# Optimization experiments

Hardware: AMD Instinct MI355X
Metric: run time of the kernel (lower is better)

Reference implementation:

```python
import jax, jax.numpy as jnp
import numpy as np

EPS = 1e-5

def _ste(x, q):
    # straight-through estimator: forward=q, backward=identity
    return x + jax.lax.stop_gradient(q - x)

def act_quant(x):
    # per-token int8 absmax quantization (BitNet b1.58 style), fake-quantized
    scale = 127.0 / jnp.clip(jnp.max(jnp.abs(x), axis=-1, keepdims=True), EPS)
    q = jnp.clip(jnp.round(x * scale), -128.0, 127.0) / scale
    return _ste(x, q)

def weight_quant(w):
    # ternary {-1,0,1} weights scaled by mean absolute value
    s = jnp.clip(jnp.mean(jnp.abs(w)), EPS)
    q = jnp.clip(jnp.round(w / s), -1.0, 1.0) * s
    return _ste(w, q)

def bit_linear(x, w):
    # x: [..., in], w: [out, in]
    return jnp.einsum('bsi,oi->bso', act_quant(x), weight_quant(w))

def setup_inputs() -> dict:
    key = jax.random.key(0)
    k1, k2, k3 = jax.random.split(key, 3)
    d_model, hidden = 2048, 4 * 2048
    x = jax.random.normal(k1, (4, 2048, d_model), dtype=jnp.float32)
    w1 = jax.random.normal(k2, (hidden, d_model), dtype=jnp.float32) * 0.02
    w2 = jax.random.normal(k3, (d_model, hidden), dtype=jnp.float32) * 0.02
    return {"x": x, "w1": w1, "w2": w2}

def reference(x, w1, w2):
    h = bit_linear(x, w1)            # [B, S, 4*d]
    h = jax.nn.gelu(h, approximate=False)  # exact erf GELU (nn.GELU default)
    return bit_linear(h, w2)         # [B, S, d]
```

## Files before the change

kernel.cpp:

```cpp
#include <hip/hip_runtime.h>
#include <hip/hip_bf16.h>
#include <hip/hip_fp16.h>
#include <stdint.h>

#define TPB 256
#define EPSF 1e-5f

using i32x4 = __attribute__((ext_vector_type(4))) int;


__device__ __forceinline__ void gload16(const void* g, void* l) {
    __builtin_amdgcn_global_load_lds(
        (__attribute__((address_space(1))) void*)g,
        (__attribute__((address_space(3))) void*)l,
        16, 0, 0);
}

__device__ __forceinline__ float wave_reduce_sum(float v) {
#pragma unroll
    for (int off = 32; off > 0; off >>= 1) v += __shfl_down(v, off, 64);
    return v;
}

__device__ __forceinline__ float wave_reduce_max(float v) {
#pragma unroll
    for (int off = 32; off > 0; off >>= 1) v = fmaxf(v, __shfl_down(v, off, 64));
    return v;
}

__device__ __forceinline__ int q8(float f, float scale, float lo, float hi) {
    return (int)fminf(fmaxf(rintf(f * scale), lo), hi);
}

__device__ __forceinline__ float gelu_fast(float x) {
    float x2 = x * x;
    float u = x * (0.7978845608f + 0.0356774081f * x2);
    float e = exp2f(u * -2.8853900817779268f);
    return x * __builtin_amdgcn_rcpf(1.0f + e);
}


__global__ void abssum2(const float* __restrict__ w1, const float* __restrict__ w2,
                        int n4, float* __restrict__ part) {
    const bool second = blockIdx.x >= 2048;
    const float4* w4 = (const float4*)(second ? w2 : w1);
    const int b = blockIdx.x & 2047;
    float acc = 0.f;
    for (int i = b * TPB + threadIdx.x; i < n4; i += 2048 * TPB) {
        float4 v = w4[i];
        acc += fabsf(v.x) + fabsf(v.y) + fabsf(v.z) + fabsf(v.w);
    }
    acc = wave_reduce_sum(acc);
    __shared__ float sh[4];
    if ((threadIdx.x & 63) == 0) sh[threadIdx.x >> 6] = acc;
    __syncthreads();
    if (threadIdx.x == 0) part[blockIdx.x] = sh[0] + sh[1] + sh[2] + sh[3];
}

__global__ void finalize_scales(const float* __restrict__ part,
                                float* __restrict__ scales, float inv_n) {
    float a = 0.f, b = 0.f;
    for (int i = threadIdx.x; i < 2048; i += TPB) { a += part[i]; b += part[i + 2048]; }
    a = wave_reduce_sum(a);
    b = wave_reduce_sum(b);
    __shared__ float sa[4], sb[4];
    if ((threadIdx.x & 63) == 0) { sa[threadIdx.x >> 6] = a; sb[threadIdx.x >> 6] = b; }
    __syncthreads();
    if (threadIdx.x == 0) {
        scales[0] = fmaxf((sa[0] + sa[1] + sa[2] + sa[3]) * inv_n, EPSF);
        scales[1] = fmaxf((sb[0] + sb[1] + sb[2] + sb[3]) * inv_n, EPSF);
    }
}


__global__ void quant_w_i8(const float* __restrict__ w,
                           signed char* __restrict__ wq,
                           const float* __restrict__ scales, int sidx, int n4) {
    const float inv = 1.0f / scales[sidx];
    const float4* w4 = (const float4*)w;
    unsigned* oq = (unsigned*)wq;
    for (int i = blockIdx.x * TPB + threadIdx.x; i < n4; i += gridDim.x * TPB) {
        float4 v = w4[i];
        unsigned p = ((unsigned)(q8(v.x, inv, -1.f, 1.f) & 0xff)) |
                     ((unsigned)(q8(v.y, inv, -1.f, 1.f) & 0xff) << 8) |
                     ((unsigned)(q8(v.z, inv, -1.f, 1.f) & 0xff) << 16) |
                     ((unsigned)(q8(v.w, inv, -1.f, 1.f) & 0xff) << 24);
        oq[i] = p;
    }
}


template <int NF4>
__global__ void quant_x_i8(const float* __restrict__ in,
                           signed char* __restrict__ outq,
                           float* __restrict__ dq, int cols) {
    const long long row = blockIdx.x;
    const float4* r4 = (const float4*)(in + row * (long long)cols);
    float4 v[NF4];
    float mx = 0.f;
#pragma unroll
    for (int j = 0; j < NF4; ++j) {
        v[j] = r4[threadIdx.x + TPB * j];
        mx = fmaxf(mx, fmaxf(fmaxf(fabsf(v[j].x), fabsf(v[j].y)),
                             fmaxf(fabsf(v[j].z), fabsf(v[j].w))));
    }
    mx = wave_reduce_max(mx);
    __shared__ float sh[4];
    __shared__ float res;
    if ((threadIdx.x & 63) == 0) sh[threadIdx.x >> 6] = mx;
    __syncthreads();
    if (threadIdx.x == 0) res = fmaxf(fmaxf(sh[0], sh[1]), fmaxf(sh[2], sh[3]));
    __syncthreads();
    const float clipped = fmaxf(res, EPSF);
    const float scale = 127.f / clipped;
    if (threadIdx.x == 0) dq[row] = clipped / 127.f;
    unsigned* oq = (unsigned*)(outq + row * (long long)cols);
#pragma unroll
    for (int j = 0; j < NF4; ++j) {
        unsigned p = ((unsigned)(q8(v[j].x, scale, -128.f, 127.f) & 0xff)) |
                     ((unsigned)(q8(v[j].y, scale, -128.f, 127.f) & 0xff) << 8) |
                     ((unsigned)(q8(v[j].z, scale, -128.f, 127.f) & 0xff) << 16) |
                     ((unsigned)(q8(v[j].w, scale, -128.f, 127.f) & 0xff) << 24);
        oq[threadIdx.x + TPB * j] = p;
    }
}


template <int NJ>
__global__ void quant_h_i8(const unsigned short* __restrict__ h,
                           signed char* __restrict__ outq,
                           float* __restrict__ dq, int cols) {
    const long long row = blockIdx.x;
    const unsigned short* rp = h + row * (long long)cols;
    uint4 v[NJ];
    float mx = 0.f;
#pragma unroll
    for (int j = 0; j < NJ; ++j) {
        v[j] = *(const uint4*)(rp + (threadIdx.x + TPB * j) * 8);
        const unsigned* u = (const unsigned*)&v[j];
#pragma unroll
        for (int e = 0; e < 4; ++e) {
            float2 f2 = __half22float2(*(const __half2*)&u[e]);
            mx = fmaxf(mx, fmaxf(fabsf(f2.x), fabsf(f2.y)));
        }
    }
    mx = wave_reduce_max(mx);
    __shared__ float sh[4];
    __shared__ float res;
    if ((threadIdx.x & 63) == 0) sh[threadIdx.x >> 6] = mx;
    __syncthreads();
    if (threadIdx.x == 0) res = fmaxf(fmaxf(sh[0], sh[1]), fmaxf(sh[2], sh[3]));
    __syncthreads();
    const float clipped = fmaxf(res, EPSF);
    const float scale = 127.f / clipped;
    if (threadIdx.x == 0) dq[row] = clipped / 127.f;
    uint2* oq = (uint2*)(outq + row * (long long)cols);
#pragma unroll
    for (int j = 0; j < NJ; ++j) {
        const unsigned* u = (const unsigned*)&v[j];
        unsigned o[2] = {0, 0};
#pragma unroll
        for (int e = 0; e < 4; ++e) {
            float2 f2 = __half22float2(*(const __half2*)&u[e]);
            unsigned b0 = (unsigned)(q8(f2.x, scale, -128.f, 127.f) & 0xff);
            unsigned b1 = (unsigned)(q8(f2.y, scale, -128.f, 127.f) & 0xff);
            o[e >> 1] |= (b0 | (b1 << 8)) << ((e & 1) * 16);
        }
        oq[threadIdx.x + TPB * j] = *(uint2*)o;
    }
}


__device__ __forceinline__ void stage_half(const char* Xb, long long rowB, int prow,
                                           int tk, char* dst, int tid, int cbs) {
    const long long gc = (long long)tk * 128 + cbs;
    const int r = tid >> 3;
    gload16(Xb + (long long)(prow + r) * rowB + gc, dst + tid * 16);
    gload16(Xb + (long long)(prow + 64 + r) * rowB + gc, dst + 8192 + tid * 16);
}

#define QUAD(MB, NB)                                                            \
    _Pragma("unroll") for (int mi = 0; mi < 4; ++mi)                            \
    _Pragma("unroll") for (int ni = 0; ni < 2; ++ni)                            \
    _Pragma("unroll") for (int ks = 0; ks < 2; ++ks)                            \
        acc[(MB)*4 + mi][(NB)*2 + ni] = __builtin_amdgcn_mfma_i32_16x16x64_i8(  \
            aq[mi][ks], bq[(NB)*2 + ni][ks], acc[(MB)*4 + mi][(NB)*2 + ni], 0, 0, 0);

#define READ_A(BUF, base_mi)                                                    \
    _Pragma("unroll") for (int mi = 0; mi < 4; ++mi) {                          \
        const char* p = (BUF) + aoff + ((mi + (base_mi)) * 16 + l15) * 128;     \
        aq[mi][0] = *(const i32x4*)(p + acb0);                                  \
        aq[mi][1] = *(const i32x4*)(p + acb1);                                  \
    }
#define READ_B(BUF, n0i, n1i)                                                   \
    _Pragma("unroll") for (int ni = (n0i); ni < (n1i); ++ni) {                  \
        const char* p = (BUF) + boff + (ni * 16 + l15) * 128;                   \
        bq[ni][0] = *(const i32x4*)(p + acb0);                                  \
        bq[ni][1] = *(const i32x4*)(p + acb1);                                  \
    }

#define LGKM(N) do { asm volatile("s_waitcnt lgkmcnt(" #N ")" ::: "memory");    \
                     __builtin_amdgcn_sched_barrier(0); } while (0)

#define EMIT1(MLO, MHI, M0V)                                                    \
    _Pragma("unroll") for (int mi = (MLO); mi < (MHI); ++mi) {                  \
        _Pragma("unroll") for (int r = 0; r < 4; ++r) {                         \
            const long long m = (M0V) + wr * 128 + mi * 16 + l4 * 4 + r;        \
            const float f = dq[m] * s;                                          \
            _Pragma("unroll") for (int ni = 0; ni < 4; ++ni) {                  \
                const long long n = n0 + wc * 64 + ni * 16 + l15;               \
                float v = gelu_fast((float)acc[mi][ni][r] * f);                 \
                __half hh = __float2half(v);                                    \
                C[m * (long long)N + n] = *(const unsigned short*)&hh;          \
                acc[mi][ni][r] = 0;                                             \
            }                                                                   \
        }                                                                       \
    }


__global__ __launch_bounds__(512, 2) void gemm1p(
    const signed char* __restrict__ A, const signed char* __restrict__ B,
    unsigned short* __restrict__ C, int N, int K,
    const float* __restrict__ dq, const float* __restrict__ scales, int ntile) {
    __shared__ __align__(16) char lds[131072];

    const int tid = threadIdx.x;
    const int lane = tid & 63;
    const int wid = tid >> 6;
    const int wr = wid >> 2;
    const int wc = wid & 3;

    const unsigned orig = blockIdx.y * gridDim.x + blockIdx.x;
    const unsigned xk = orig & 7, j = orig >> 3;
    const unsigned bx = xk * 4 + (j & 3);
    const unsigned byg = j >> 2;

    const int n0 = (int)bx * 256;
    const long long rb = (long long)K;
    const char* Ab = (const char*)A;
    const char* Bb = (const char*)B;

    const int NTT = ntile << 4;

    const int cbs = (((tid & 7) ^ ((tid >> 3) & 7)) << 4);
    const int l15 = lane & 15, l4 = lane >> 4;
    const int swz = (lane & 7) << 4;
    const int acb0 = (l4 * 16) ^ swz;
    const int acb1 = (64 + l4 * 16) ^ swz;
    const int aoff = wr * 16384;
    const int boff = 32768 + (wc >> 1) * 16384 + (wc & 1) * 8192;

    i32x4 acc[8][4] = {};
    i32x4 aq[4][2], bq[4][2];

    auto mrow = [&](int v) -> int { return ((int)byg * ntile + (v >> 4)) * 256; };

    stage_half(Bb, rb, n0, 0, lds + 32768, tid, cbs);
    stage_half(Bb, rb, n0 + 128, 0, lds + 32768 + 16384, tid, cbs);
    stage_half(Ab, rb, mrow(0), 0, lds + 0, tid, cbs);
    stage_half(Ab, rb, mrow(0) + 128, 0, lds + 16384, tid, cbs);
    stage_half(Bb, rb, n0, 1, lds + 65536 + 32768, tid, cbs);
    stage_half(Bb, rb, n0 + 128, 1, lds + 65536 + 32768 + 16384, tid, cbs);
    stage_half(Ab, rb, mrow(1), 1, lds + 65536, tid, cbs);
    asm volatile("s_waitcnt vmcnt(6)" ::: "memory");
    __builtin_amdgcn_sched_barrier(0);
    __builtin_amdgcn_s_barrier();
    READ_A(lds, 0);
    READ_B(lds, 0, 2);

    const float s = scales[0];

    for (int vt = 0; vt < NTT; ++vt) {
        char* cur = lds + ((vt & 1) << 16);
        char* nxt = lds + (((vt + 1) & 1) << 16);
        const bool s1 = (vt + 1) < NTT;
        const bool s2 = (vt + 2) < NTT;
        const int kk = vt & 15;
        const int k1 = (vt + 1) & 15;
        const int k2 = (vt + 2) & 15;

        if (s1) stage_half(Ab, rb, mrow(vt + 1) + 128, k1, nxt + 16384, tid, cbs);
        READ_B(cur, 2, 4);
        if (kk == 0 && vt > 0) { EMIT1(4, 8, mrow(vt - 1)); }
        __builtin_amdgcn_s_barrier();
        LGKM(4);
        __builtin_amdgcn_s_setprio(1);
        QUAD(0, 0);
        __builtin_amdgcn_s_setprio(0);

        __builtin_amdgcn_s_barrier();
        LGKM(0);
        __builtin_amdgcn_s_setprio(1);
        QUAD(0, 1);
        __builtin_amdgcn_s_setprio(0);

        if (s2) {
            stage_half(Bb, rb, n0, k2, cur + 32768, tid, cbs);
            stage_half(Bb, rb, n0 + 128, k2, cur + 32768 + 16384, tid, cbs);
        }
        READ_A(cur, 4);
        if (kk == 15) { EMIT1(0, 4, mrow(vt)); }
        __builtin_amdgcn_s_barrier();
        LGKM(0);
        __builtin_amdgcn_s_setprio(1);
        QUAD(1, 0);
        __builtin_amdgcn_s_setprio(0);

        if (s2) { asm volatile("s_waitcnt vmcnt(4)" ::: "memory"); }
        else    { asm volatile("s_waitcnt vmcnt(0)" ::: "memory"); }
        __builtin_amdgcn_sched_barrier(0);
        __builtin_amdgcn_s_barrier();
        if (s2) stage_half(Ab, rb, mrow(vt + 2), k2, cur, tid, cbs);
        __builtin_amdgcn_s_setprio(1);
        QUAD(1, 1);
        __builtin_amdgcn_s_setprio(0);
        if (s1) {
            READ_A(nxt, 0);
            READ_B(nxt, 0, 2);
        }
    }

    { EMIT1(4, 8, mrow(NTT - 1)); }
}


#define EMIT2(MLO, MHI)                                                         \
    _Pragma("unroll") for (int mi = (MLO); mi < (MHI); ++mi) {                  \
        _Pragma("unroll") for (int r = 0; r < 4; ++r) {                         \
            const long long m = M0 + wr * 128 + mi * 16 + l4 * 4 + r;           \
            const float f = dq[m] * s;                                          \
            _Pragma("unroll") for (int ni = 0; ni < 4; ++ni) {                  \
                const long long n = N0 + wc * 64 + ni * 16 + l15;               \
                __builtin_nontemporal_store(                                    \
                    (float)acc[mi][ni][r] * f, C + m * (long long)N + n);       \
            }                                                                   \
        }                                                                       \
    }

__global__ __launch_bounds__(512, 2) void gemm2k(
    const signed char* __restrict__ A, const signed char* __restrict__ B,
    float* __restrict__ C, int N, int K,
    const float* __restrict__ dq, const float* __restrict__ scales) {
    __shared__ __align__(16) char lds[131072];

    const int tid = threadIdx.x;
    const int lane = tid & 63;
    const int wid = tid >> 6;
    const int wr = wid >> 2;
    const int wc = wid & 3;

    const unsigned gx = gridDim.x;
    unsigned lin = blockIdx.y * gx + blockIdx.x;
    const unsigned qq = (gx * gridDim.y) >> 3;
    lin = (lin & 7) * qq + (lin >> 3);
    const unsigned bx = lin % gx;
    const unsigned by = lin / gx;

    const long long M0 = (long long)by * 256;
    const long long N0 = (long long)bx * 256;
    const long long rb = (long long)K;
    const char* Ab = (const char*)A + M0 * rb;
    const char* Bb = (const char*)B + N0 * rb;
    const int nt = K >> 7;

    const int cbs = (((tid & 7) ^ ((tid >> 3) & 7)) << 4);
    const int l15 = lane & 15, l4 = lane >> 4;
    const int swz = (lane & 7) << 4;
    const int acb0 = (l4 * 16) ^ swz;
    const int acb1 = (64 + l4 * 16) ^ swz;
    const int aoff = wr * 16384;
    const int boff = 32768 + (wc >> 1) * 16384 + (wc & 1) * 8192;

    i32x4 acc[8][4] = {};
    i32x4 aq[4][2], bq[4][2];

    stage_half(Bb, rb, 0,   0, lds + 32768,         tid, cbs);
    stage_half(Bb, rb, 128, 0, lds + 32768 + 16384, tid, cbs);
    stage_half(Ab, rb, 0,   0, lds + 0,             tid, cbs);
    stage_half(Ab, rb, 128, 0, lds + 16384,         tid, cbs);
    stage_half(Bb, rb, 0,   1, lds + 65536 + 32768,         tid, cbs);
    stage_half(Bb, rb, 128, 1, lds + 65536 + 32768 + 16384, tid, cbs);
    stage_half(Ab, rb, 0,   1, lds + 65536,                 tid, cbs);
    asm volatile("s_waitcnt vmcnt(6)" ::: "memory");
    __builtin_amdgcn_sched_barrier(0);
    __builtin_amdgcn_s_barrier();
    READ_A(lds, 0);
    READ_B(lds, 0, 2);

    const float s = scales[1];

    for (int t = 0; t < nt; ++t) {
        char* cur = lds + ((t & 1) << 16);
        char* nxt = lds + (((t + 1) & 1) << 16);
        const bool s1 = (t + 1) < nt;
        const bool s2 = (t + 2) < nt;

        if (s1) stage_half(Ab, rb, 128, t + 1, nxt + 16384, tid, cbs);
        READ_B(cur, 2, 4);
        __builtin_amdgcn_s_barrier();
        LGKM(4);
        __builtin_amdgcn_s_setprio(1);
        QUAD(0, 0);
        __builtin_amdgcn_s_setprio(0);

        __builtin_amdgcn_s_barrier();
        LGKM(0);
        __builtin_amdgcn_s_setprio(1);
        QUAD(0, 1);
        __builtin_amdgcn_s_setprio(0);

        if (s2) {
            stage_half(Bb, rb, 0, t + 2, cur + 32768, tid, cbs);
            stage_half(Bb, rb, 128, t + 2, cur + 32768 + 16384, tid, cbs);
        }
        READ_A(cur, 4);
        if (t == nt - 1) { EMIT2(0, 4); }
        __builtin_amdgcn_s_barrier();
        LGKM(0);
        __builtin_amdgcn_s_setprio(1);
        QUAD(1, 0);
        __builtin_amdgcn_s_setprio(0);

        if (s2) { asm volatile("s_waitcnt vmcnt(4)" ::: "memory"); }
        else    { asm volatile("s_waitcnt vmcnt(0)" ::: "memory"); }
        __builtin_amdgcn_sched_barrier(0);
        __builtin_amdgcn_s_barrier();
        if (s2) stage_half(Ab, rb, 0, t + 2, cur, tid, cbs);
        __builtin_amdgcn_s_setprio(1);
        QUAD(1, 1);
        __builtin_amdgcn_s_setprio(0);
        if (s1) {
            READ_A(nxt, 0);
            READ_B(nxt, 0, 2);
        }
    }

    { EMIT2(4, 8); }
}


extern "C" void kernel_launch(void* const* d_in, const int* in_sizes, int n_in,
                              void* d_out, int out_size, void* d_ws, size_t ws_size,
                              hipStream_t stream) {
    (void)n_in; (void)out_size;
    const float* x  = (const float*)d_in[0];
    const float* w1 = (const float*)d_in[1];
    const float* w2 = (const float*)d_in[2];
    float* out = (float*)d_out;

    const int D = 2048, H = 8192;
    const long long M = (long long)in_sizes[0] / D;

    char* base = (char*)d_ws;
    size_t off = 0;
    auto alloc = [&](size_t bytes) -> char* {
        char* r = base + off;
        off = (off + bytes + 255) & ~(size_t)255;
        return r;
    };

    const bool fullM = ws_size >= (size_t)236 * 1024 * 1024;
    const long long MC = fullM ? M : M / 2;

    float* part = (float*)alloc(4096 * 4);
    float* scales = (float*)alloc(256);
    float* dqx = (float*)alloc((size_t)M * 4);
    float* dqh = (float*)alloc((size_t)M * 4);
    signed char* wq = (signed char*)alloc((size_t)H * D);
    signed char* xq = (signed char*)alloc((size_t)M * D);
    signed char* hq = (signed char*)alloc((size_t)M * H);
    unsigned short* hf = (unsigned short*)alloc((size_t)MC * H * 2);

    const int nw4 = H * D / 4;
    abssum2<<<4096, TPB, 0, stream>>>(w1, w2, nw4, part);
    finalize_scales<<<1, TPB, 0, stream>>>(part, scales, 1.0f / (float)(H * D));
    quant_w_i8<<<2048, TPB, 0, stream>>>(w1, wq, scales, 0, nw4);
    quant_x_i8<2><<<(int)M, TPB, 0, stream>>>(x, xq, dqx, D);

    if (fullM) {
        gemm1p<<<dim3(32, 8), 512, 0, stream>>>(xq, wq, hf, H, D, dqx, scales, 4);
        quant_h_i8<4><<<(int)M, TPB, 0, stream>>>(hf, hq, dqh, H);
    } else {
        for (int g = 0; g < 2; ++g) {
            const long long m0 = g * MC;
            gemm1p<<<dim3(32, 8), 512, 0, stream>>>(
                xq + m0 * D, wq, hf, H, D, dqx + m0, scales, 2);
            quant_h_i8<4><<<(int)MC, TPB, 0, stream>>>(hf, hq + m0 * H, dqh + m0, H);
        }
    }

    quant_w_i8<<<2048, TPB, 0, stream>>>(w2, wq, scales, 1, nw4);

    gemm2k<<<dim3(D / 256, (int)(M / 256)), 512, 0, stream>>>(
        hq, wq, out, D, H, dqh, scales);
}
```

Baseline: 357.7 us.

## Move GELU into h-quant kernel and store packed permuted GEMM1 outputs

The GEMM1 epilogue now writes four adjacent fp16 values per row as one 8-byte store instead of four scattered 2-byte stores, and no longer applies GELU. GELU is instead applied in the per-row h quantization kernel, which keeps the GELU values in registers for the absmax and quantize passes. Because the stored h columns are permuted within 16-column groups, w2 is quantized with a matching lane-shuffle permutation so the GEMM2 reduction stays consistent. This removes uncoalesced epilogue writes, at the cost of extra shuffles in w2 quantization, more registers in quant_h, and a result that depends on the two permutations matching exactly.

```diff
diff --git a/kernel.cpp b/kernel.cpp
--- a/kernel.cpp
+++ b/kernel.cpp
@@ -90,6 +90,32 @@
 }
 
 
+__global__ void quant_w2_i8perm(const float* __restrict__ w,
+                                signed char* __restrict__ wq,
+                                const float* __restrict__ scales, int n4) {
+    const float inv = 1.0f / scales[1];
+    const float4* w4 = (const float4*)w;
+    unsigned* oq = (unsigned*)wq;
+    const int t = threadIdx.x;
+    const int g = t & 15;
+    const int srcbase = (t & ~15);
+    for (int i = blockIdx.x * TPB + t; i < n4; i += gridDim.x * TPB) {
+        float4 v = w4[i];
+        unsigned p = ((unsigned)(q8(v.x, inv, -1.f, 1.f) & 0xff)) |
+                     ((unsigned)(q8(v.y, inv, -1.f, 1.f) & 0xff) << 8) |
+                     ((unsigned)(q8(v.z, inv, -1.f, 1.f) & 0xff) << 16) |
+                     ((unsigned)(q8(v.w, inv, -1.f, 1.f) & 0xff) << 24);
+        unsigned out = 0;
+#pragma unroll
+        for (int j = 0; j < 4; ++j) {
+            unsigned pj = (unsigned)__shfl((int)p, srcbase + 4 * j + (g >> 2), 64);
+            out |= ((pj >> ((g & 3) * 8)) & 0xffu) << (8 * j);
+        }
+        oq[i] = out;
+    }
+}
+
+
 template <int NF4>
 __global__ void quant_x_i8(const float* __restrict__ in,
                            signed char* __restrict__ outq,
@@ -132,16 +158,20 @@
                            float* __restrict__ dq, int cols) {
     const long long row = blockIdx.x;
     const unsigned short* rp = h + row * (long long)cols;
-    uint4 v[NJ];
+    float g[NJ * 8];
     float mx = 0.f;
 #pragma unroll
     for (int j = 0; j < NJ; ++j) {
-        v[j] = *(const uint4*)(rp + (threadIdx.x + TPB * j) * 8);
-        const unsigned* u = (const unsigned*)&v[j];
+        uint4 v = *(const uint4*)(rp + (threadIdx.x + TPB * j) * 8);
+        const unsigned* u = (const unsigned*)&v;
 #pragma unroll
         for (int e = 0; e < 4; ++e) {
             float2 f2 = __half22float2(*(const __half2*)&u[e]);
-            mx = fmaxf(mx, fmaxf(fabsf(f2.x), fabsf(f2.y)));
+            float g0 = gelu_fast(f2.x);
+            float g1 = gelu_fast(f2.y);
+            g[j * 8 + 2 * e] = g0;
+            g[j * 8 + 2 * e + 1] = g1;
+            mx = fmaxf(mx, fmaxf(fabsf(g0), fabsf(g1)));
         }
     }
     mx = wave_reduce_max(mx);
@@ -157,14 +187,11 @@
     uint2* oq = (uint2*)(outq + row * (long long)cols);
 #pragma unroll
     for (int j = 0; j < NJ; ++j) {
-        const unsigned* u = (const unsigned*)&v[j];
         unsigned o[2] = {0, 0};
 #pragma unroll
-        for (int e = 0; e < 4; ++e) {
-            float2 f2 = __half22float2(*(const __half2*)&u[e]);
-            unsigned b0 = (unsigned)(q8(f2.x, scale, -128.f, 127.f) & 0xff);
-            unsigned b1 = (unsigned)(q8(f2.y, scale, -128.f, 127.f) & 0xff);
-            o[e >> 1] |= (b0 | (b1 << 8)) << ((e & 1) * 16);
+        for (int e = 0; e < 8; ++e) {
+            unsigned b = (unsigned)(q8(g[j * 8 + e], scale, -128.f, 127.f) & 0xff);
+            o[e >> 2] |= b << ((e & 3) * 8);
         }
         oq[threadIdx.x + TPB * j] = *(uint2*)o;
     }
@@ -207,13 +234,16 @@
         _Pragma("unroll") for (int r = 0; r < 4; ++r) {                         \
             const long long m = (M0V) + wr * 128 + mi * 16 + l4 * 4 + r;        \
             const float f = dq[m] * s;                                          \
-            _Pragma("unroll") for (int ni = 0; ni < 4; ++ni) {                  \
-                const long long n = n0 + wc * 64 + ni * 16 + l15;               \
-                float v = gelu_fast((float)acc[mi][ni][r] * f);                 \
-                __half hh = __float2half(v);                                    \
-                C[m * (long long)N + n] = *(const unsigned short*)&hh;          \
-                acc[mi][ni][r] = 0;                                             \
-            }                                                                   \
+            __half2 lo = __floats2half2_rn((float)acc[mi][0][r] * f,            \
+                                           (float)acc[mi][1][r] * f);           \
+            __half2 hi = __floats2half2_rn((float)acc[mi][2][r] * f,            \
+                                           (float)acc[mi][3][r] * f);           \
+            uint2 pk;                                                           \
+            pk.x = *(const unsigned*)&lo;                                       \
+            pk.y = *(const unsigned*)&hi;                                       \
+            *(uint2*)(C + m * (long long)N + n0 + wc * 64 + l15 * 4) = pk;      \
+            acc[mi][0][r] = 0; acc[mi][1][r] = 0;                               \
+            acc[mi][2][r] = 0; acc[mi][3][r] = 0;                               \
         }                                                                       \
     }
 
@@ -489,7 +519,7 @@
         }
     }
 
-    quant_w_i8<<<2048, TPB, 0, stream>>>(w2, wq, scales, 1, nw4);
+    quant_w2_i8perm<<<2048, TPB, 0, stream>>>(w2, wq, scales, nw4);
 
     gemm2k<<<dim3(D / 256, (int)(M / 256)), 512, 0, stream>>>(
         hq, wq, out, D, H, dqh, scales);
```

Result: faster. 349.4 us, median of 3 (-2.3%).
